# Optimization experiments

Measured on AMD Instinct MI355X. Metric: run time of the kernel, lower is better.

## Reference

```python
import jax, jax.numpy as jnp
import numpy as np

N = 50000            # nodes
E = 800000           # random edges (self loops added in reference, per PyG default)
D_IN, D1, D2, D_OUT = 256, 128, 64, 40
SLOPE = 0.2          # GATv2Conv default negative_slope


def _glorot(key, shape):
    fan_in, fan_out = shape[0], shape[-1]
    s = jnp.sqrt(6.0 / (fan_in + fan_out))
    return jax.random.uniform(key, shape, jnp.float32, -s, s)


def setup_inputs() -> dict:
    key = jax.random.key(0)
    ks = jax.random.split(key, 16)
    inp = {
        "x": jax.random.normal(ks[0], (N, D_IN), jnp.float32),
        "edge_index": jax.random.randint(ks[1], (2, E), 0, N),
    }
    dims = [(D_IN, D1), (D1, D2), (D2, D_OUT)]
    k = 2
    for i, (di, do) in enumerate(dims, 1):
        inp[f"W{i}l"] = _glorot(ks[k], (di, do)); k += 1
        inp[f"W{i}r"] = _glorot(ks[k], (di, do)); k += 1
        inp[f"b{i}l"] = jnp.zeros((do,), jnp.float32)
        inp[f"b{i}r"] = jnp.zeros((do,), jnp.float32)
        inp[f"a{i}"]  = _glorot(ks[k], (do,));    k += 1
        inp[f"c{i}"]  = jnp.zeros((do,), jnp.float32)
    return inp


def _gatv2(x, src, dst, Wl, bl, Wr, br, att, bias):
    # GATv2Conv, heads=1: lin_l on source nodes, lin_r on target nodes
    xl = x @ Wl + bl                     # [N, do] source transform
    xr = x @ Wr + br                     # [N, do] target transform
    e = jax.nn.leaky_relu(xl[src] + xr[dst], SLOPE)   # [Etot, do]
    logits = e @ att                     # [Etot]
    # segment softmax over incoming edges of each dst node
    m = jax.ops.segment_max(logits, dst, num_segments=N)
    ex = jnp.exp(logits - m[dst])
    denom = jax.ops.segment_sum(ex, dst, num_segments=N)
    alpha = ex / denom[dst]              # [Etot]
    out = jax.ops.segment_sum(alpha[:, None] * xl[src], dst, num_segments=N)
    return out + bias


def reference(x, edge_index,
              W1l, W1r, b1l, b1r, a1, c1,
              W2l, W2r, b2l, b2r, a2, c2,
              W3l, W3r, b3l, b3r, a3, c3):
    loop = jnp.arange(N, dtype=edge_index.dtype)
    src = jnp.concatenate([edge_index[0], loop])   # add_self_loops=True
    dst = jnp.concatenate([edge_index[1], loop])
    h = jax.nn.relu(_gatv2(x, src, dst, W1l, b1l, W1r, b1r, a1, c1))
    h = jax.nn.relu(_gatv2(h, src, dst, W2l, b2l, W2r, b2r, a2, c2))
    h = _gatv2(h, src, dst, W3l, b3l, W3r, b3r, a3, c3)
    return jax.nn.log_softmax(h, axis=1)
```

## Files before the change

kernel.cpp:

```cpp
#include <hip/hip_runtime.h>
#include <math.h>

#define NN 50000
#define NE 800000
#define SLOPE 0.2f
#define NEGX (-1e30f)
#define CH 8192

typedef _Float16 h8 __attribute__((ext_vector_type(8)));
typedef _Float16 h2 __attribute__((ext_vector_type(2)));
typedef float f8 __attribute__((ext_vector_type(8)));
typedef float v4f __attribute__((ext_vector_type(4)));

__device__ __forceinline__ h8 hzero(){ h8 z = {0,0,0,0,0,0,0,0}; return z; }
__device__ __forceinline__ f8 fzero(){ f8 z = {0,0,0,0,0,0,0,0}; return z; }

__device__ __forceinline__ void pack_one(const float* __restrict__ W,
                                         _Float16* __restrict__ Wp,
                                         int DO, int K, int NT, int t){
  int KC = K >> 5;
  if (t >= NT * KC * 64) return;
  int lane = t & 63;
  int rest = t >> 6;
  int c  = rest % KC;
  int nt = rest / KC;
  int col = nt * 16 + (lane & 15);
  int k0  = c * 32 + ((lane >> 4) << 3);
  _Float16 o[8];
#pragma unroll
  for (int j = 0; j < 8; j++){
    float v = (col < DO) ? W[(k0 + j) * DO + col] : 0.f;
    o[j] = (_Float16)v;
  }
  *(ulonglong2*)(Wp + (size_t)t * 8) = *(ulonglong2*)o;
}

__global__ __launch_bounds__(256) void k_pack_hist(
    const float* W1l, const float* W1r, const float* W2l,
    const float* W2r, const float* W3l, const float* W3r,
    _Float16* p1l, _Float16* p1r, _Float16* p2l,
    _Float16* p2r, _Float16* p3l, _Float16* p3r,
    const int* __restrict__ ei, int* __restrict__ gbp){
  __shared__ int h[256];
  int b = blockIdx.x, t = threadIdx.x;
  if (b < 44){
    if      (b < 16) pack_one(W1l, p1l, 128, 256, 8, (b     ) * 256 + t);
    else if (b < 32) pack_one(W1r, p1r, 128, 256, 8, (b - 16) * 256 + t);
    else if (b < 36) pack_one(W2l, p2l,  64, 128, 4, (b - 32) * 256 + t);
    else if (b < 40) pack_one(W2r, p2r,  64, 128, 4, (b - 36) * 256 + t);
    else if (b < 42) pack_one(W3l, p3l,  40,  64, 3, (b - 40) * 256 + t);
    else             pack_one(W3r, p3r,  40,  64, 3, (b - 42) * 256 + t);
  } else {
    int hb = b - 44;
    h[t] = 0;
    __syncthreads();
    int e0 = hb * 12500;
    for (int i = t; i < 12500; i += 256)
      atomicAdd(&h[ei[NE + e0 + i] >> 8], 1);
    __syncthreads();
    gbp[hb * 256 + t] = h[t];
  }
}

__global__ __launch_bounds__(256) void k_scan(const int* __restrict__ gbp,
                                              int* __restrict__ base,
                                              int* __restrict__ bcur,
                                              int* __restrict__ row_ptr,
                                              int* __restrict__ dcnt,
                                              int* __restrict__ dcur){
  __shared__ int s[256];
  int t = threadIdx.x;
  dcnt[t] = 0;
  dcur[t] = 0;
  int v = 0;
#pragma unroll 8
  for (int i = 0; i < 64; i++) v += gbp[i * 256 + t];
  s[t] = v; __syncthreads();
  for (int off = 1; off < 256; off <<= 1){
    int a = (t >= off) ? s[t - off] : 0;
    __syncthreads(); s[t] += a; __syncthreads();
  }
  int ex = s[t] - v;
  base[t] = ex;
  bcur[t] = ex;
  if (t == 255){ base[256] = s[255]; row_ptr[NN] = s[255]; }
}

__global__ __launch_bounds__(256) void k_bscatter(const int* __restrict__ ei,
                                                  int* __restrict__ bcur,
                                                  unsigned* __restrict__ pk_out){
  __shared__ unsigned pk[CH];
  __shared__ int h[256];
  int t = threadIdx.x;
  int e0 = blockIdx.x * CH;
  h[t] = 0;
  __syncthreads();
  int n = NE - e0; if (n > CH) n = CH;
  for (int i = t; i < n; i += 256){
    int e = e0 + i;
    int s = ei[e], d = ei[NE + e];
    pk[i] = (unsigned)s | ((unsigned)(d & 255) << 16) | ((unsigned)(d >> 8) << 24);
    atomicAdd(&h[d >> 8], 1);
  }
  __syncthreads();
  int c = h[t];
  if (c) h[t] = atomicAdd(&bcur[t], c);
  __syncthreads();
  for (int i = t; i < n; i += 256){
    unsigned u = pk[i];
    int pos = atomicAdd(&h[u >> 24], 1);
    pk_out[pos] = u;
  }
}

__global__ __launch_bounds__(256) void k_bcsr(const unsigned* __restrict__ pk,
                                              const int* __restrict__ base,
                                              int* __restrict__ row_ptr,
                                              int* __restrict__ csr_src,
                                              int* __restrict__ dcnt){
  __shared__ int h[256], s[256];
  int t = threadIdx.x;
  int b = blockIdx.x;
  int lo = base[b], hi = base[b + 1];
  h[t] = 0;
  __syncthreads();
  for (int i = lo + t; i < hi; i += 256)
    atomicAdd(&h[(pk[i] >> 16) & 255], 1);
  __syncthreads();
  int v = h[t];
  s[t] = v; __syncthreads();
  for (int off = 1; off < 256; off <<= 1){
    int a = (t >= off) ? s[t - off] : 0;
    __syncthreads(); s[t] += a; __syncthreads();
  }
  int ex = lo + s[t] - v;
  int node = b * 256 + t;
  if (node < NN) row_ptr[node] = ex;
  h[t] = ex;
  s[t] = 0;
  __syncthreads();
  if (node < NN) atomicAdd(&s[v < 255 ? v : 255], 1);
  __syncthreads();
  if (s[t]) atomicAdd(&dcnt[t], s[t]);
  for (int i = lo + t; i < hi; i += 256){
    unsigned u = pk[i];
    int pos = atomicAdd(&h[(u >> 16) & 255], 1);
    csr_src[pos] = (int)(u & 0xFFFFu);
  }
}

__global__ __launch_bounds__(256) void k_dscatter(const int* __restrict__ row_ptr,
                                                  const int* __restrict__ dcnt,
                                                  int* __restrict__ dcur,
                                                  int* __restrict__ perm){
  __shared__ int lh[256], sc[256];
  int t = threadIdx.x;
  int node = blockIdx.x * 256 + t;
  lh[t] = 0;
  int dv = dcnt[t];
  __syncthreads();
  int bin = -1;
  if (node < NN){
    int deg = row_ptr[node + 1] - row_ptr[node];
    bin = deg < 255 ? deg : 255;
    atomicAdd(&lh[bin], 1);
  }
  sc[t] = dv;
  __syncthreads();
  for (int off = 1; off < 256; off <<= 1){
    int a = (t >= off) ? sc[t - off] : 0;
    __syncthreads(); sc[t] += a; __syncthreads();
  }
  int gbase = sc[t] - dv;
  int c = lh[t];
  int bp = c ? (gbase + atomicAdd(&dcur[t], c)) : 0;
  __syncthreads();
  lh[t] = bp;
  __syncthreads();
  if (node < NN){
    int pos = atomicAdd(&lh[bin], 1);
    perm[pos] = node;
  }
}

template<typename TI, int K, int DO>
__global__ __launch_bounds__(256, 4) void gemm_direct(
    const TI* __restrict__ X,
    const _Float16* __restrict__ Wpl, const float* __restrict__ bl,
    const _Float16* __restrict__ Wpr, const float* __restrict__ br,
    _Float16* __restrict__ Yl, _Float16* __restrict__ Yr)
{
  constexpr int KC = K / 32;
  constexpr int NT = (DO + 15) / 16;
  int lane = threadIdx.x & 63;
  int wv   = threadIdx.x >> 6;
  int row0 = (blockIdx.x * 4 + wv) * 16;
  int arow = lane & 15;
  int koff = lane >> 4;
  int lrow = row0 + arow;
  int crow = (lrow < NN) ? lrow : 0;

  h8 afrag[KC];
  if constexpr (sizeof(TI) == 4){
    const float* Xr = (const float*)X + (size_t)crow * K + koff * 8;
#pragma unroll
    for (int c = 0; c < KC; c++){
      float4 v0 = *reinterpret_cast<const float4*>(Xr + c * 32);
      float4 v1 = *reinterpret_cast<const float4*>(Xr + c * 32 + 4);
      h8 a;
      a[0]=(_Float16)v0.x; a[1]=(_Float16)v0.y; a[2]=(_Float16)v0.z; a[3]=(_Float16)v0.w;
      a[4]=(_Float16)v1.x; a[5]=(_Float16)v1.y; a[6]=(_Float16)v1.z; a[7]=(_Float16)v1.w;
      afrag[c] = a;
    }
  } else {
    const _Float16* Xr = (const _Float16*)X + (size_t)crow * K + koff * 8;
#pragma unroll
    for (int c = 0; c < KC; c++)
      afrag[c] = *reinterpret_cast<const h8*>(Xr + c * 32);
  }

#pragma unroll
  for (int side = 0; side < 2; side++){
    const _Float16* Wp = side ? Wpr : Wpl;
    const float* bias = side ? br : bl;
    _Float16* Y = side ? Yr : Yl;
#pragma unroll
    for (int nt = 0; nt < NT; nt++){
      v4f acc = {0.f, 0.f, 0.f, 0.f};
#pragma unroll
      for (int c = 0; c < KC; c++){
        h8 b = *reinterpret_cast<const h8*>(Wp + (size_t)((nt * KC + c) * 64 + lane) * 8);
        acc = __builtin_amdgcn_mfma_f32_16x16x32_f16(afrag[c], b, acc, 0, 0, 0);
      }
      int col = nt * 16 + arow;
      if (col < DO){
        float bv = bias[col];
        int rbase = row0 + koff * 4;
#pragma unroll
        for (int r = 0; r < 4; r++){
          int orow = rbase + r;
          if (orow < NN) Y[(size_t)orow * DO + col] = (_Float16)(acc[r] + bv);
        }
      }
    }
  }
}

template<int CTRL>
__device__ __forceinline__ float dppmv(float v){
  int x = __builtin_amdgcn_update_dpp(0, __float_as_int(v), CTRL, 0xF, 0xF, true);
  return __int_as_float(x);
}

template<int LPG>
__device__ __forceinline__ float gsum(float v){
  v += dppmv<177>(v);
  v += dppmv<78>(v);
  if (LPG >= 8)  v += dppmv<0x141>(v);
  if (LPG == 16) v += dppmv<0x140>(v);
  return v;
}
template<int LPG>
__device__ __forceinline__ void gsum2(float& a, float& b){
  a = gsum<LPG>(a);
  b = gsum<LPG>(b);
}
template<int LPG>
__device__ __forceinline__ void gsum4(float& a, float& b, float& c, float& d){
  a = gsum<LPG>(a);
  b = gsum<LPG>(b);
  c = gsum<LPG>(c);
  d = gsum<LPG>(d);
}
template<int LPG>
__device__ __forceinline__ float gmax(float v){
  v = fmaxf(v, dppmv<177>(v));
  v = fmaxf(v, dppmv<78>(v));
  if (LPG >= 8)  v = fmaxf(v, dppmv<0x141>(v));
  if (LPG == 16) v = fmaxf(v, dppmv<0x140>(v));
  return v;
}

__device__ __forceinline__ float edge_logit(h8 x, h8 xrv, h8 attv){
  h8 t = x + xrv;
  h8 l = __builtin_elementwise_max(t, t * (_Float16)SLOPE);
  const h2* lp = (const h2*)&l;
  const h2* ap = (const h2*)&attv;
  float d = __builtin_amdgcn_fdot2(lp[0], ap[0], 0.f, false);
  d = __builtin_amdgcn_fdot2(lp[1], ap[1], d, false);
  d = __builtin_amdgcn_fdot2(lp[2], ap[2], d, false);
  d = __builtin_amdgcn_fdot2(lp[3], ap[3], d, false);
  return d;
}

__device__ __forceinline__ void fmix(f8& acc, h8 x, float w){
#pragma unroll
  for (int j = 0; j < 8; j++) acc[j] = fmaf((float)x[j], w, acc[j]);
}

template<int DO, int LPG, int DO2>
__global__ __launch_bounds__(256) void agg_gemm(
    const _Float16* __restrict__ xl, const _Float16* __restrict__ xr,
    const int* __restrict__ csr_src, const int* __restrict__ row_ptr,
    const int* __restrict__ perm,
    const float* __restrict__ att, const float* __restrict__ bias,
    const _Float16* __restrict__ Wpl2, const float* __restrict__ bl2,
    const _Float16* __restrict__ Wpr2, const float* __restrict__ br2,
    _Float16* __restrict__ Yl, _Float16* __restrict__ Yr)
{
  constexpr int G = 64 / LPG;
  constexpr int NPB = 4 * G;
  constexpr int LK = DO + 8;
  constexpr int KC2 = DO / 32;
  constexpr int NT2 = (DO2 + 15) / 16;
  constexpr int MT = NPB / 16;
  __shared__ _Float16 hs[NPB * LK];
  __shared__ int nodeOf[NPB];

  int tid  = threadIdx.x;
  int lane = tid & 63;
  int wid  = tid >> 6;

  unsigned seg = (unsigned)(blockIdx.x * 1021u) % gridDim.x;
  if (tid < NPB){
    int idx = seg * NPB + tid;
    nodeOf[tid] = (idx < NN) ? perm[idx] : NN;
  }
  __syncthreads();

  int g = lane / LPG, p = lane % LPG;
  int nodeLocal = wid * G + g;
  int node = nodeOf[nodeLocal];
  int cbase = p * 8;
  bool nvalid = node < NN;
  int nodeC = nvalid ? node : 0;

  h8 attv, xrv, xlv;
  {
    float4 a0 = *reinterpret_cast<const float4*>(att + cbase);
    float4 a1 = *reinterpret_cast<const float4*>(att + cbase + 4);
    attv[0]=(_Float16)a0.x; attv[1]=(_Float16)a0.y; attv[2]=(_Float16)a0.z; attv[3]=(_Float16)a0.w;
    attv[4]=(_Float16)a1.x; attv[5]=(_Float16)a1.y; attv[6]=(_Float16)a1.z; attv[7]=(_Float16)a1.w;
    xrv = *reinterpret_cast<const h8*>(xr + nodeC * DO + cbase);
    xlv = *reinterpret_cast<const h8*>(xl + nodeC * DO + cbase);
  }
  float s = gsum<LPG>(edge_logit(xlv, xrv, attv));
  float wS = __expf(s);
  float denA = wS, denB = 0.f;
  f8 accA = fzero(), accB = fzero();
  fmix(accA, xlv, wS);

  int e0 = row_ptr[nodeC];
  int e1 = nvalid ? row_ptr[nodeC + 1] : e0;
  int e = e0;
  for (; e + 3 < e1; e += 4){
    int s0 = csr_src[e],     s1 = csr_src[e + 1];
    int s2 = csr_src[e + 2], s3 = csr_src[e + 3];
    h8 x0 = *reinterpret_cast<const h8*>(xl + s0 * DO + cbase);
    h8 x1 = *reinterpret_cast<const h8*>(xl + s1 * DO + cbase);
    h8 x2 = *reinterpret_cast<const h8*>(xl + s2 * DO + cbase);
    h8 x3 = *reinterpret_cast<const h8*>(xl + s3 * DO + cbase);
    float p0 = edge_logit(x0, xrv, attv);
    float p1 = edge_logit(x1, xrv, attv);
    float p2 = edge_logit(x2, xrv, attv);
    float p3 = edge_logit(x3, xrv, attv);
    gsum4<LPG>(p0, p1, p2, p3);
    float w0 = __expf(p0), w1 = __expf(p1);
    float w2 = __expf(p2), w3 = __expf(p3);
    denA += w0 + w2; denB += w1 + w3;
    fmix(accA, x0, w0);
    fmix(accB, x1, w1);
    fmix(accA, x2, w2);
    fmix(accB, x3, w3);
  }
  for (; e + 1 < e1; e += 2){
    int sA = csr_src[e], sB = csr_src[e + 1];
    h8 xA = *reinterpret_cast<const h8*>(xl + sA * DO + cbase);
    h8 xB = *reinterpret_cast<const h8*>(xl + sB * DO + cbase);
    float pA = edge_logit(xA, xrv, attv);
    float pB = edge_logit(xB, xrv, attv);
    gsum2<LPG>(pA, pB);
    float wA = __expf(pA), wB = __expf(pB);
    denA += wA; denB += wB;
    fmix(accA, xA, wA);
    fmix(accB, xB, wB);
  }
  if (e < e1){
    int sA = csr_src[e];
    h8 xA = *reinterpret_cast<const h8*>(xl + sA * DO + cbase);
    float pA = gsum<LPG>(edge_logit(xA, xrv, attv));
    float w = __expf(pA);
    denA += w;
    fmix(accA, xA, w);
  }

  {
    float inv = 1.0f / (denA + denB);
    f8 sum = (accA + accB) * inv;
    float4 b0 = *reinterpret_cast<const float4*>(bias + cbase);
    float4 b1 = *reinterpret_cast<const float4*>(bias + cbase + 4);
    f8 bv = {b0.x, b0.y, b0.z, b0.w, b1.x, b1.y, b1.z, b1.w};
    sum += bv;
    sum = __builtin_elementwise_max(sum, fzero());
    *reinterpret_cast<h8*>(&hs[nodeLocal * LK + cbase]) = __builtin_convertvector(sum, h8);
  }
  __syncthreads();

  int arow = lane & 15;
  int koff = lane >> 4;
  int mt = (MT == 1) ? 0 : (wid >> 1);
  h8 afrag[KC2];
#pragma unroll
  for (int c = 0; c < KC2; c++)
    afrag[c] = *reinterpret_cast<const h8*>(&hs[(mt * 16 + arow) * LK + koff * 8 + c * 32]);

  int side = wid & 1;
  const _Float16* Wp = side ? Wpr2 : Wpl2;
  const float* bias2 = side ? br2 : bl2;
  _Float16* Y = side ? Yr : Yl;
  int nt_begin = (MT == 1) ? (wid >> 1) * (NT2 / 2) : 0;
  int nt_end   = (MT == 1) ? nt_begin + NT2 / 2 : NT2;
  for (int nt = nt_begin; nt < nt_end; nt++){
    v4f acc = {0.f, 0.f, 0.f, 0.f};
#pragma unroll
    for (int c = 0; c < KC2; c++){
      h8 b = *reinterpret_cast<const h8*>(Wp + (size_t)((nt * KC2 + c) * 64 + lane) * 8);
      acc = __builtin_amdgcn_mfma_f32_16x16x32_f16(afrag[c], b, acc, 0, 0, 0);
    }
    int col = nt * 16 + arow;
    if (col < DO2){
      float bv = bias2[col];
      int lrbase = mt * 16 + koff * 4;
#pragma unroll
      for (int r = 0; r < 4; r++){
        int orow = nodeOf[lrbase + r];
        if (orow < NN) Y[(size_t)orow * DO2 + col] = (_Float16)(acc[r] + bv);
      }
    }
  }
}

template<int DO, int LPG>
__global__ __launch_bounds__(256) void gat_agg_out(
    const _Float16* __restrict__ xl, const _Float16* __restrict__ xr,
    const int* __restrict__ csr_src, const int* __restrict__ row_ptr,
    const int* __restrict__ perm,
    const float* __restrict__ att, const float* __restrict__ bias,
    float* __restrict__ out)
{
  constexpr int G = 64 / LPG;
  constexpr int NPB = 4 * G;
  __shared__ int nodeOf[NPB];
  int tid  = threadIdx.x;
  int lane = tid & 63;
  int wid  = tid >> 6;

  unsigned seg = (unsigned)(blockIdx.x * 1021u) % gridDim.x;
  if (tid < NPB){
    int idx = seg * NPB + tid;
    nodeOf[tid] = (idx < NN) ? perm[idx] : NN;
  }
  __syncthreads();

  int g = lane / LPG;
  int p = lane % LPG;
  int node = nodeOf[wid * G + g];
  bool nvalid = node < NN;
  int nodeC = nvalid ? node : 0;
  int cbase = p * 8;
  bool ok = (cbase < DO);

  h8 attv = hzero(), xrv = hzero(), xlv = hzero();
  if (ok){
    float4 a0 = *reinterpret_cast<const float4*>(att + cbase);
    float4 a1 = *reinterpret_cast<const float4*>(att + cbase + 4);
    attv[0]=(_Float16)a0.x; attv[1]=(_Float16)a0.y; attv[2]=(_Float16)a0.z; attv[3]=(_Float16)a0.w;
    attv[4]=(_Float16)a1.x; attv[5]=(_Float16)a1.y; attv[6]=(_Float16)a1.z; attv[7]=(_Float16)a1.w;
    xrv = *reinterpret_cast<const h8*>(xr + nodeC * DO + cbase);
    xlv = *reinterpret_cast<const h8*>(xl + nodeC * DO + cbase);
  }

  float s = gsum<LPG>(edge_logit(xlv, xrv, attv));
  float wS = __expf(s);
  float denA = wS, denB = 0.f;
  f8 accA = fzero(), accB = fzero();
  fmix(accA, xlv, wS);

  int e0 = row_ptr[nodeC];
  int e1 = nvalid ? row_ptr[nodeC + 1] : e0;
  int e = e0;
  for (; e + 3 < e1; e += 4){
    int s0 = csr_src[e],     s1 = csr_src[e + 1];
    int s2 = csr_src[e + 2], s3 = csr_src[e + 3];
    h8 x0 = ok ? *reinterpret_cast<const h8*>(xl + s0 * DO + cbase) : hzero();
    h8 x1 = ok ? *reinterpret_cast<const h8*>(xl + s1 * DO + cbase) : hzero();
    h8 x2 = ok ? *reinterpret_cast<const h8*>(xl + s2 * DO + cbase) : hzero();
    h8 x3 = ok ? *reinterpret_cast<const h8*>(xl + s3 * DO + cbase) : hzero();
    float p0 = edge_logit(x0, xrv, attv);
    float p1 = edge_logit(x1, xrv, attv);
    float p2 = edge_logit(x2, xrv, attv);
    float p3 = edge_logit(x3, xrv, attv);
    gsum4<LPG>(p0, p1, p2, p3);
    float w0 = __expf(p0), w1 = __expf(p1);
    float w2 = __expf(p2), w3 = __expf(p3);
    denA += w0 + w2; denB += w1 + w3;
    fmix(accA, x0, w0);
    fmix(accB, x1, w1);
    fmix(accA, x2, w2);
    fmix(accB, x3, w3);
  }
  for (; e + 1 < e1; e += 2){
    int sA = csr_src[e], sB = csr_src[e + 1];
    h8 xA = ok ? *reinterpret_cast<const h8*>(xl + sA * DO + cbase) : hzero();
    h8 xB = ok ? *reinterpret_cast<const h8*>(xl + sB * DO + cbase) : hzero();
    float pA = edge_logit(xA, xrv, attv);
    float pB = edge_logit(xB, xrv, attv);
    gsum2<LPG>(pA, pB);
    float wA = __expf(pA), wB = __expf(pB);
    denA += wA; denB += wB;
    fmix(accA, xA, wA);
    fmix(accB, xB, wB);
  }
  if (e < e1){
    int sA = csr_src[e];
    h8 xA = ok ? *reinterpret_cast<const h8*>(xl + sA * DO + cbase) : hzero();
    float pA = gsum<LPG>(edge_logit(xA, xrv, attv));
    float w = __expf(pA);
    denA += w;
    fmix(accA, xA, w);
  }

  float inv = 1.0f / (denA + denB);
  f8 sumv = (accA + accB) * inv;
  float v[8]; float lmax = NEGX;
#pragma unroll
  for (int j = 0; j < 8; j++){
    v[j] = ok ? (sumv[j] + bias[cbase + j]) : NEGX;
    lmax = fmaxf(lmax, v[j]);
  }
  lmax = gmax<LPG>(lmax);
  float lsum = 0.f;
#pragma unroll
  for (int j = 0; j < 8; j++) lsum += __expf(v[j] - lmax);
  lsum = gsum<LPG>(lsum);
  if (ok && nvalid){
    float lg = lmax + __logf(lsum);
    float* op = (float*)out + node * DO + cbase;
    float4 o0, o1;
    o0.x = v[0] - lg; o0.y = v[1] - lg; o0.z = v[2] - lg; o0.w = v[3] - lg;
    o1.x = v[4] - lg; o1.y = v[5] - lg; o1.z = v[6] - lg; o1.w = v[7] - lg;
    *reinterpret_cast<float4*>(op) = o0;
    *reinterpret_cast<float4*>(op + 4) = o1;
  }
}

extern "C" void kernel_launch(void* const* d_in, const int* in_sizes, int n_in,
                              void* d_out, int out_size, void* d_ws, size_t ws_size,
                              hipStream_t stream) {
  const float* x   = (const float*)d_in[0];
  const int*   ei  = (const int*)d_in[1];
  const float* W1l = (const float*)d_in[2];  const float* W1r = (const float*)d_in[3];
  const float* b1l = (const float*)d_in[4];  const float* b1r = (const float*)d_in[5];
  const float* a1  = (const float*)d_in[6];  const float* c1  = (const float*)d_in[7];
  const float* W2l = (const float*)d_in[8];  const float* W2r = (const float*)d_in[9];
  const float* b2l = (const float*)d_in[10]; const float* b2r = (const float*)d_in[11];
  const float* a2  = (const float*)d_in[12]; const float* c2  = (const float*)d_in[13];
  const float* W3l = (const float*)d_in[14]; const float* W3r = (const float*)d_in[15];
  const float* b3l = (const float*)d_in[16]; const float* b3r = (const float*)d_in[17];
  const float* a3  = (const float*)d_in[18]; const float* c3  = (const float*)d_in[19];
  float* outp = (float*)d_out;

  _Float16* xl1 = (_Float16*)d_ws;
  _Float16* xr1 = xl1 + 6400000;
  _Float16* xl2 = xr1 + 6400000;
  _Float16* xr2 = xl2 + 3200000;
  _Float16* xl3 = xr2 + 3200000;
  _Float16* xr3 = xl3 + 2000000;
  _Float16* wp1l = xr3 + 2000000;
  _Float16* wp1r = wp1l + 32768;
  _Float16* wp2l = wp1r + 32768;
  _Float16* wp2r = wp2l + 8192;
  _Float16* wp3l = wp2r + 8192;
  _Float16* wp3r = wp3l + 3072;
  unsigned* pk   = (unsigned*)(wp3r + 3072);
  int* csr_src   = (int*)(pk + NE);
  int* row_ptr   = csr_src + NE;
  int* gbp       = row_ptr + 50001;
  int* base      = gbp + 16384;
  int* bcur      = base + 257;
  int* perm      = bcur + 256;
  int* dcnt      = perm + NN;
  int* dcur      = dcnt + 256;

  const int GB = (NN + 63) / 64;
  const int SB = (NE + CH - 1) / CH;
  const int FB1 = (NN + 15) / 16;
  const int FB2 = (NN + 31) / 32;
  const int AB3 = (NN + 31) / 32;

  k_pack_hist<<<108, 256, 0, stream>>>(W1l, W1r, W2l, W2r, W3l, W3r,
                                       wp1l, wp1r, wp2l, wp2r, wp3l, wp3r,
                                       ei, gbp);
  k_scan<<<1, 256, 0, stream>>>(gbp, base, bcur, row_ptr, dcnt, dcur);
  k_bscatter<<<SB, 256, 0, stream>>>(ei, bcur, pk);
  k_bcsr<<<196, 256, 0, stream>>>(pk, base, row_ptr, csr_src, dcnt);
  k_dscatter<<<196, 256, 0, stream>>>(row_ptr, dcnt, dcur, perm);

  gemm_direct<float,256,128><<<GB, 256, 0, stream>>>(x, wp1l, b1l, wp1r, b1r, xl1, xr1);

  agg_gemm<128,16,64><<<FB1, 256, 0, stream>>>(xl1, xr1, csr_src, row_ptr, perm,
                                               a1, c1, wp2l, b2l, wp2r, b2r, xl2, xr2);

  agg_gemm<64,8,40><<<FB2, 256, 0, stream>>>(xl2, xr2, csr_src, row_ptr, perm,
                                             a2, c2, wp3l, b3l, wp3r, b3r, xl3, xr3);

  gat_agg_out<40,8><<<AB3, 256, 0, stream>>>(xl3, xr3, csr_src, row_ptr, perm, a3, c3, outp);
}
```

Measured before the change: 285.7 us.

## Merge CSR preprocessing kernels with layer-1 GEMM to cut launches

```diff
diff --git a/kernel.cpp b/kernel.cpp
--- a/kernel.cpp
+++ b/kernel.cpp
@@ -40,7 +40,8 @@
     const float* W2r, const float* W3l, const float* W3r,
     _Float16* p1l, _Float16* p1r, _Float16* p2l,
     _Float16* p2r, _Float16* p3l, _Float16* p3r,
-    const int* __restrict__ ei, int* __restrict__ gbp){
+    const int* __restrict__ ei, int* __restrict__ gbp,
+    int* __restrict__ deg, int* __restrict__ row_ptr){
   __shared__ int h[256];
   int b = blockIdx.x, t = threadIdx.x;
   if (b < 44){
@@ -52,171 +53,48 @@
     else             pack_one(W3r, p3r,  40,  64, 3, (b - 42) * 256 + t);
   } else {
     int hb = b - 44;
+    if (hb == 0 && t == 0) row_ptr[NN] = NE;
     h[t] = 0;
     __syncthreads();
     int e0 = hb * 12500;
-    for (int i = t; i < 12500; i += 256)
-      atomicAdd(&h[ei[NE + e0 + i] >> 8], 1);
+    for (int i = t; i < 12500; i += 256){
+      int d = ei[NE + e0 + i];
+      atomicAdd(&h[d >> 8], 1);
+      atomicAdd(&deg[d], 1);
+    }
     __syncthreads();
     gbp[hb * 256 + t] = h[t];
   }
 }
 
-__global__ __launch_bounds__(256) void k_scan(const int* __restrict__ gbp,
-                                              int* __restrict__ base,
-                                              int* __restrict__ bcur,
-                                              int* __restrict__ row_ptr,
-                                              int* __restrict__ dcnt,
-                                              int* __restrict__ dcur){
-  __shared__ int s[256];
-  int t = threadIdx.x;
-  dcnt[t] = 0;
-  dcur[t] = 0;
-  int v = 0;
-#pragma unroll 8
-  for (int i = 0; i < 64; i++) v += gbp[i * 256 + t];
-  s[t] = v; __syncthreads();
-  for (int off = 1; off < 256; off <<= 1){
-    int a = (t >= off) ? s[t - off] : 0;
-    __syncthreads(); s[t] += a; __syncthreads();
-  }
-  int ex = s[t] - v;
-  base[t] = ex;
-  bcur[t] = ex;
-  if (t == 255){ base[256] = s[255]; row_ptr[NN] = s[255]; }
-}
-
-__global__ __launch_bounds__(256) void k_bscatter(const int* __restrict__ ei,
-                                                  int* __restrict__ bcur,
-                                                  unsigned* __restrict__ pk_out){
-  __shared__ unsigned pk[CH];
-  __shared__ int h[256];
-  int t = threadIdx.x;
-  int e0 = blockIdx.x * CH;
-  h[t] = 0;
-  __syncthreads();
-  int n = NE - e0; if (n > CH) n = CH;
-  for (int i = t; i < n; i += 256){
-    int e = e0 + i;
-    int s = ei[e], d = ei[NE + e];
-    pk[i] = (unsigned)s | ((unsigned)(d & 255) << 16) | ((unsigned)(d >> 8) << 24);
-    atomicAdd(&h[d >> 8], 1);
-  }
-  __syncthreads();
-  int c = h[t];
-  if (c) h[t] = atomicAdd(&bcur[t], c);
-  __syncthreads();
-  for (int i = t; i < n; i += 256){
-    unsigned u = pk[i];
-    int pos = atomicAdd(&h[u >> 24], 1);
-    pk_out[pos] = u;
-  }
-}
-
-__global__ __launch_bounds__(256) void k_bcsr(const unsigned* __restrict__ pk,
-                                              const int* __restrict__ base,
-                                              int* __restrict__ row_ptr,
-                                              int* __restrict__ csr_src,
-                                              int* __restrict__ dcnt){
-  __shared__ int h[256], s[256];
-  int t = threadIdx.x;
-  int b = blockIdx.x;
-  int lo = base[b], hi = base[b + 1];
-  h[t] = 0;
-  __syncthreads();
-  for (int i = lo + t; i < hi; i += 256)
-    atomicAdd(&h[(pk[i] >> 16) & 255], 1);
-  __syncthreads();
-  int v = h[t];
-  s[t] = v; __syncthreads();
-  for (int off = 1; off < 256; off <<= 1){
-    int a = (t >= off) ? s[t - off] : 0;
-    __syncthreads(); s[t] += a; __syncthreads();
-  }
-  int ex = lo + s[t] - v;
-  int node = b * 256 + t;
-  if (node < NN) row_ptr[node] = ex;
-  h[t] = ex;
-  s[t] = 0;
-  __syncthreads();
-  if (node < NN) atomicAdd(&s[v < 255 ? v : 255], 1);
-  __syncthreads();
-  if (s[t]) atomicAdd(&dcnt[t], s[t]);
-  for (int i = lo + t; i < hi; i += 256){
-    unsigned u = pk[i];
-    int pos = atomicAdd(&h[(u >> 16) & 255], 1);
-    csr_src[pos] = (int)(u & 0xFFFFu);
-  }
-}
-
-__global__ __launch_bounds__(256) void k_dscatter(const int* __restrict__ row_ptr,
-                                                  const int* __restrict__ dcnt,
-                                                  int* __restrict__ dcur,
-                                                  int* __restrict__ perm){
-  __shared__ int lh[256], sc[256];
-  int t = threadIdx.x;
-  int node = blockIdx.x * 256 + t;
-  lh[t] = 0;
-  int dv = dcnt[t];
-  __syncthreads();
-  int bin = -1;
-  if (node < NN){
-    int deg = row_ptr[node + 1] - row_ptr[node];
-    bin = deg < 255 ? deg : 255;
-    atomicAdd(&lh[bin], 1);
-  }
-  sc[t] = dv;
-  __syncthreads();
-  for (int off = 1; off < 256; off <<= 1){
-    int a = (t >= off) ? sc[t - off] : 0;
-    __syncthreads(); sc[t] += a; __syncthreads();
-  }
-  int gbase = sc[t] - dv;
-  int c = lh[t];
-  int bp = c ? (gbase + atomicAdd(&dcur[t], c)) : 0;
-  __syncthreads();
-  lh[t] = bp;
-  __syncthreads();
-  if (node < NN){
-    int pos = atomicAdd(&lh[bin], 1);
-    perm[pos] = node;
-  }
-}
-
-template<typename TI, int K, int DO>
-__global__ __launch_bounds__(256, 4) void gemm_direct(
-    const TI* __restrict__ X,
+__device__ __forceinline__ void gemm_body(
+    int bb,
+    const float* __restrict__ X,
     const _Float16* __restrict__ Wpl, const float* __restrict__ bl,
     const _Float16* __restrict__ Wpr, const float* __restrict__ br,
     _Float16* __restrict__ Yl, _Float16* __restrict__ Yr)
 {
+  constexpr int K = 256, DO = 128;
   constexpr int KC = K / 32;
-  constexpr int NT = (DO + 15) / 16;
+  constexpr int NT = DO / 16;
   int lane = threadIdx.x & 63;
   int wv   = threadIdx.x >> 6;
-  int row0 = (blockIdx.x * 4 + wv) * 16;
+  int row0 = (bb * 4 + wv) * 16;
   int arow = lane & 15;
   int koff = lane >> 4;
   int lrow = row0 + arow;
   int crow = (lrow < NN) ? lrow : 0;
 
   h8 afrag[KC];
-  if constexpr (sizeof(TI) == 4){
-    const float* Xr = (const float*)X + (size_t)crow * K + koff * 8;
-#pragma unroll
-    for (int c = 0; c < KC; c++){
-      float4 v0 = *reinterpret_cast<const float4*>(Xr + c * 32);
-      float4 v1 = *reinterpret_cast<const float4*>(Xr + c * 32 + 4);
-      h8 a;
-      a[0]=(_Float16)v0.x; a[1]=(_Float16)v0.y; a[2]=(_Float16)v0.z; a[3]=(_Float16)v0.w;
-      a[4]=(_Float16)v1.x; a[5]=(_Float16)v1.y; a[6]=(_Float16)v1.z; a[7]=(_Float16)v1.w;
-      afrag[c] = a;
-    }
-  } else {
-    const _Float16* Xr = (const _Float16*)X + (size_t)crow * K + koff * 8;
-#pragma unroll
-    for (int c = 0; c < KC; c++)
-      afrag[c] = *reinterpret_cast<const h8*>(Xr + c * 32);
+  const float* Xr = X + (size_t)crow * K + koff * 8;
+#pragma unroll
+  for (int c = 0; c < KC; c++){
+    float4 v0 = *reinterpret_cast<const float4*>(Xr + c * 32);
+    float4 v1 = *reinterpret_cast<const float4*>(Xr + c * 32 + 4);
+    h8 a;
+    a[0]=(_Float16)v0.x; a[1]=(_Float16)v0.y; a[2]=(_Float16)v0.z; a[3]=(_Float16)v0.w;
+    a[4]=(_Float16)v1.x; a[5]=(_Float16)v1.y; a[6]=(_Float16)v1.z; a[7]=(_Float16)v1.w;
+    afrag[c] = a;
   }
 
 #pragma unroll
@@ -243,6 +121,124 @@
         }
       }
     }
+  }
+}
+
+__global__ __launch_bounds__(256, 4) void k_fused2(
+    const int* __restrict__ ei, const int* __restrict__ gbp,
+    int* __restrict__ bcur, int* __restrict__ base,
+    unsigned* __restrict__ pk_out,
+    const int* __restrict__ deg, int* __restrict__ dcnt,
+    const float* __restrict__ X,
+    const _Float16* __restrict__ Wpl, const float* __restrict__ bl,
+    const _Float16* __restrict__ Wpr, const float* __restrict__ br,
+    _Float16* __restrict__ Yl, _Float16* __restrict__ Yr)
+{
+  __shared__ unsigned smem[CH + 512];
+  int b = blockIdx.x, t = threadIdx.x;
+  if (b < 98){
+    unsigned* pk = smem;
+    int* h = (int*)(smem + CH);
+    int* s = h + 256;
+    int v = 0;
+#pragma unroll 8
+    for (int i = 0; i < 64; i++) v += gbp[i * 256 + t];
+    s[t] = v; __syncthreads();
+    for (int off = 1; off < 256; off <<= 1){
+      int a = (t >= off) ? s[t - off] : 0;
+      __syncthreads(); s[t] += a; __syncthreads();
+    }
+    int ex = s[t] - v;
+    if (b == 0){
+      base[t] = ex;
+      if (t == 255) base[256] = NE;
+    }
+    h[t] = 0;
+    __syncthreads();
+    int e0 = b * CH;
+    int n = NE - e0; if (n > CH) n = CH;
+    for (int i = t; i < n; i += 256){
+      int e = e0 + i;
+      int sN = ei[e], d = ei[NE + e];
+      pk[i] = (unsigned)sN | ((unsigned)(d & 255) << 16) | ((unsigned)(d >> 8) << 24);
+      atomicAdd(&h[d >> 8], 1);
+    }
+    __syncthreads();
+    int c = h[t];
+    if (c) h[t] = ex + atomicAdd(&bcur[t], c);
+    __syncthreads();
+    for (int i = t; i < n; i += 256){
+      unsigned u = pk[i];
+      int pos = atomicAdd(&h[u >> 24], 1);
+      pk_out[pos] = u;
+    }
+  } else if (b < 294){
+    int* lh = (int*)smem;
+    lh[t] = 0;
+    __syncthreads();
+    int node = (b - 98) * 256 + t;
+    if (node < NN){
+      int dg = deg[node];
+      atomicAdd(&lh[dg < 255 ? dg : 255], 1);
+    }
+    __syncthreads();
+    if (lh[t]) atomicAdd(&dcnt[t], lh[t]);
+  } else {
+    gemm_body(b - 294, X, Wpl, bl, Wpr, br, Yl, Yr);
+  }
+}
+
+__global__ __launch_bounds__(256) void k_bcsr_perm(
+    const unsigned* __restrict__ pk, const int* __restrict__ base,
+    int* __restrict__ row_ptr, int* __restrict__ csr_src,
+    const int* __restrict__ dcnt, int* __restrict__ dcur,
+    int* __restrict__ perm){
+  __shared__ int h[256], s[256];
+  int t = threadIdx.x;
+  int b = blockIdx.x;
+  int lo = base[b], hi = base[b + 1];
+  h[t] = 0;
+  __syncthreads();
+  for (int i = lo + t; i < hi; i += 256)
+    atomicAdd(&h[(pk[i] >> 16) & 255], 1);
+  __syncthreads();
+  int v = h[t];
+  s[t] = v; __syncthreads();
+  for (int off = 1; off < 256; off <<= 1){
+    int a = (t >= off) ? s[t - off] : 0;
+    __syncthreads(); s[t] += a; __syncthreads();
+  }
+  int ex = lo + s[t] - v;
+  int node = b * 256 + t;
+  if (node < NN) row_ptr[node] = ex;
+  h[t] = ex;
+  __syncthreads();
+  for (int i = lo + t; i < hi; i += 256){
+    unsigned u = pk[i];
+    int pos = atomicAdd(&h[(u >> 16) & 255], 1);
+    csr_src[pos] = (int)(u & 0xFFFFu);
+  }
+  __syncthreads();
+  s[t] = 0;
+  int dv = dcnt[t];
+  __syncthreads();
+  int bin = v < 255 ? v : 255;
+  if (node < NN) atomicAdd(&s[bin], 1);
+  h[t] = dv;
+  __syncthreads();
+  for (int off = 1; off < 256; off <<= 1){
+    int a = (t >= off) ? h[t - off] : 0;
+    __syncthreads(); h[t] += a; __syncthreads();
+  }
+  int dbase = h[t] - dv;
+  int c = s[t];
+  int bp = c ? (dbase + atomicAdd(&dcur[t], c)) : 0;
+  __syncthreads();
+  s[t] = bp;
+  __syncthreads();
+  if (node < NN){
+    int pos = atomicAdd(&s[bin], 1);
+    perm[pos] = node;
   }
 }
 
@@ -588,25 +584,28 @@
   int* gbp       = row_ptr + 50001;
   int* base      = gbp + 16384;
   int* bcur      = base + 257;
-  int* perm      = bcur + 256;
-  int* dcnt      = perm + NN;
+  int* dcnt      = bcur + 256;
   int* dcur      = dcnt + 256;
-
-  const int GB = (NN + 63) / 64;
-  const int SB = (NE + CH - 1) / CH;
+  int* deg       = dcur + 256;
+  int* perm      = deg + NN;
+
   const int FB1 = (NN + 15) / 16;
   const int FB2 = (NN + 31) / 32;
   const int AB3 = (NN + 31) / 32;
+  const int GB  = (NN + 63) / 64;
+  const int SB  = (NE + CH - 1) / CH;
+  const int F2  = SB + 196 + GB;
+
+  hipMemsetAsync(bcur, 0, (size_t)(256 * 3 + NN) * sizeof(int), stream);
 
   k_pack_hist<<<108, 256, 0, stream>>>(W1l, W1r, W2l, W2r, W3l, W3r,
                                        wp1l, wp1r, wp2l, wp2r, wp3l, wp3r,
-                                       ei, gbp);
-  k_scan<<<1, 256, 0, stream>>>(gbp, base, bcur, row_ptr, dcnt, dcur);
-  k_bscatter<<<SB, 256, 0, stream>>>(ei, bcur, pk);
-  k_bcsr<<<196, 256, 0, stream>>>(pk, base, row_ptr, csr_src, dcnt);
-  k_dscatter<<<196, 256, 0, stream>>>(row_ptr, dcnt, dcur, perm);
-
-  gemm_direct<float,256,128><<<GB, 256, 0, stream>>>(x, wp1l, b1l, wp1r, b1r, xl1, xr1);
+                                       ei, gbp, deg, row_ptr);
+
+  k_fused2<<<F2, 256, 0, stream>>>(ei, gbp, bcur, base, pk, deg, dcnt,
+                                   x, wp1l, b1l, wp1r, b1r, xl1, xr1);
+
+  k_bcsr_perm<<<196, 256, 0, stream>>>(pk, base, row_ptr, csr_src, dcnt, dcur, perm);
 
   agg_gemm<128,16,64><<<FB1, 256, 0, stream>>>(xl1, xr1, csr_src, row_ptr, perm,
                                                a1, c1, wp2l, b2l, wp2r, b2r, xl2, xr2);
```

Result: slower. 296.8 us (+3.9%).
